# Performance work log

Hardware: AMD Instinct MI355X
Metric: run time of the kernel (lower is better)

The kernel has to match this reference:

```python
import jax, jax.numpy as jnp
import numpy as np

EPS = 1e-5  # BatchNorm eps (eval mode, running_mean=0, running_var=1)


def conv1x1(x, w):
    # x: [n,c,h,w], w: [o,c]
    return jnp.einsum('nchw,oc->nohw', x, w)


def bn_relu(x, s, b):
    scale = s / jnp.sqrt(1.0 + EPS)
    return jax.nn.relu(x * scale[None, :, None, None] + b[None, :, None, None])


def upsample_bilinear_ac(x, out_h, out_w):
    # nn.Upsample(mode='bilinear', align_corners=True)
    n, c, h, w = x.shape
    ys = jnp.linspace(0.0, h - 1.0, out_h)
    xs = jnp.linspace(0.0, w - 1.0, out_w)
    y0 = jnp.floor(ys).astype(jnp.int32)
    y1 = jnp.minimum(y0 + 1, h - 1)
    x0 = jnp.floor(xs).astype(jnp.int32)
    x1 = jnp.minimum(x0 + 1, w - 1)
    wy = (ys - y0)[None, None, :, None]
    wx = (xs - x0)[None, None, None, :]
    rows = x[:, :, y0, :] * (1.0 - wy) + x[:, :, y1, :] * wy
    return rows[:, :, :, x0] * (1.0 - wx) + rows[:, :, :, x1] * wx


def to_patches(x, ph, pw):
    # [n,c,H,W] -> [n,c,P,L], P = (H//ph)*(W//pw) patches, L = ph*pw pixels
    n, c, H, W = x.shape
    gh, gw = H // ph, W // pw
    return x.reshape(n, c, gh, ph, gw, pw).transpose(0, 1, 2, 4, 3, 5).reshape(n, c, gh * gw, ph * pw)


def from_patches(x, H, W, ph, pw):
    n, c, P, L = x.shape
    gh, gw = H // ph, W // pw
    return x.reshape(n, c, gh, gw, ph, pw).transpose(0, 1, 2, 4, 3, 5).reshape(n, c, H, W)


def patch_attention(q, k, v, ph, pw, H, W):
    qp = to_patches(q, ph, pw)
    kp = to_patches(k, ph, pw)
    vp = to_patches(v, ph, pw)
    # patch-vs-patch similarity, contracted over pixels within a patch
    sim = jax.nn.sigmoid(jnp.einsum('ncpl,ncql->ncpq', qp, kp))
    # sim1 (mean over key patches) + sim2 (mean over query patches), both [n,c,P,1]
    gate = sim.mean(axis=3, keepdims=True) + sim.mean(axis=2)[..., None]
    return from_patches(gate * vp, H, W, ph, pw)


def setup_inputs() -> dict:
    key = jax.random.key(0)
    ks = jax.random.split(key, 20)
    N, Ch, Cl, neck = 8, 256, 512, 64
    H = W = 128
    Hs = Ws = 32
    sc = 0.05
    return {
        'branch0_feats': jax.random.normal(ks[0], (N, Ch, H, W), jnp.float32),
        'other_feats': jax.random.normal(ks[1], (N, Cl, Hs, Ws), jnp.float32),
        'wq1': jax.random.normal(ks[2], (neck, Ch), jnp.float32) * sc,
        'bnq1_s': jax.random.uniform(ks[3], (neck,), jnp.float32, 0.5, 1.5),
        'bnq1_b': jax.random.normal(ks[4], (neck,), jnp.float32) * 0.1,
        'wk1': jax.random.normal(ks[5], (neck, Cl), jnp.float32) * sc,
        'bnk1_s': jax.random.uniform(ks[6], (neck,), jnp.float32, 0.5, 1.5),
        'bnk1_b': jax.random.normal(ks[7], (neck,), jnp.float32) * 0.1,
        'wv1': jax.random.normal(ks[8], (neck, Ch), jnp.float32) * sc,
        'wq2': jax.random.normal(ks[9], (neck, Ch), jnp.float32) * sc,
        'bnq2_s': jax.random.uniform(ks[10], (neck,), jnp.float32, 0.5, 1.5),
        'bnq2_b': jax.random.normal(ks[11], (neck,), jnp.float32) * 0.1,
        'wk2': jax.random.normal(ks[12], (neck, Cl), jnp.float32) * sc,
        'bnk2_s': jax.random.uniform(ks[13], (neck,), jnp.float32, 0.5, 1.5),
        'bnk2_b': jax.random.normal(ks[14], (neck,), jnp.float32) * 0.1,
        'wz': jax.random.normal(ks[15], (Ch, 2 * neck), jnp.float32) * sc,
        'alpha': jax.random.uniform(ks[16], (1,), jnp.float32),
        'gamma': jax.random.uniform(ks[17], (1,), jnp.float32),
    }


def reference(branch0_feats, other_feats, wq1, bnq1_s, bnq1_b, wk1, bnk1_s, bnk1_b, wv1,
              wq2, bnq2_s, bnq2_b, wk2, bnk2_s, bnk2_b, wz, alpha, gamma):
    _, _, H, W = branch0_feats.shape
    _, _, Hs, Ws = other_feats.shape

    value = conv1x1(branch0_feats, wv1)
    query = bn_relu(conv1x1(branch0_feats, wq1), bnq1_s, bnq1_b)
    key = upsample_bilinear_ac(bn_relu(conv1x1(other_feats, wk1), bnk1_s, bnk1_b), H, W)

    half = query.shape[1] // 2
    # scale 1: patches of size (Hs, Ws)
    ctx0 = patch_attention(query[:, :half], key[:, :half], value[:, :half], Hs, Ws, H, W)
    # scale 2: patches of size (Hs//2, Ws//2)
    ctx2 = patch_attention(query[:, half:], key[:, half:], value[:, half:], Hs // 2, Ws // 2, H, W)

    # dense per-pixel sigmoid gating branch
    query2 = bn_relu(conv1x1(branch0_feats, wq2), bnq2_s, bnq2_b)
    key2 = upsample_bilinear_ac(bn_relu(conv1x1(other_feats, wk2), bnk2_s, bnk2_b), H, W)
    ctx3 = value * jax.nn.sigmoid(query2 * key2)

    context = jnp.concatenate([alpha[0] * jnp.concatenate([ctx0, ctx2], axis=1),
                               gamma[0] * ctx3], axis=1)
    return conv1x1(context, wz)
```

## Files before the change

### kernel.cpp

```cpp
#include <hip/hip_runtime.h>
#include <hip/hip_bf16.h>
#include <math.h>
#include <stdint.h>

#define N_    8
#define CH    256
#define CL    512
#define NECK  64
#define H_    128
#define W_    128
#define HW    16384
#define HWS   1024
#define EPSB  1e-5f
#define SC31  (31.0f/127.0f)

typedef unsigned short ushort_t;
typedef __attribute__((ext_vector_type(8))) short bf16x8;
typedef __attribute__((ext_vector_type(4))) float f32x4;

union bfpack { ushort_t u[8]; bf16x8 v; };

__device__ __forceinline__ float sigmoidf_(float x){ return 1.0f/(1.0f + __expf(-x)); }

__device__ __forceinline__ ushort_t f2bf(float x){
    union { __hip_bfloat16 h; ushort_t u; } cv;
    cv.h = __float2bfloat16(x);
    return cv.u;
}
__device__ __forceinline__ uint32_t pack2(float lo, float hi){
    return (uint32_t)f2bf(lo) | ((uint32_t)f2bf(hi) << 16);
}
__device__ __forceinline__ float bf2f(ushort_t b){
    union { uint32_t u; float f; } v; v.u = ((uint32_t)b) << 16;
    return v.f;
}

__global__ __launch_bounds__(512) void k_phase1(
    const float* __restrict__ x,
    const float* __restrict__ xo,
    const float* __restrict__ wv1, const float* __restrict__ wq1, const float* __restrict__ wq2,
    const float* __restrict__ wk1, const float* __restrict__ wk2,
    const float* __restrict__ s1, const float* __restrict__ b1,
    const float* __restrict__ s2, const float* __restrict__ b2,
    const float* __restrict__ sk1, const float* __restrict__ bk1,
    const float* __restrict__ sk2, const float* __restrict__ bk2,
    const float* __restrict__ wz,
    ushort_t* __restrict__ value, ushort_t* __restrict__ query, ushort_t* __restrict__ query2,
    float* __restrict__ k1s, float* __restrict__ k2s, ushort_t* __restrict__ Wzb)
{
    __shared__ __align__(16) char smem[40960];
    int blk = blockIdx.x;
    int t = threadIdx.x;

    if (blk >= 1088){
        int i = (blk - 1088)*2048 + t*4;
        float4 f = *(const float4*)(wz + i);
        *(uint2*)(Wzb + i) = make_uint2(pack2(f.x,f.y), pack2(f.z,f.w));
        return;
    }

    int lane = t & 63, w8 = t >> 6;
    int wm = w8 >> 1, wn = w8 & 1;
    int r16 = lane & 15;
    float inv = rsqrtf(1.0f + EPSB);

    if (blk >= 1024){
        ushort_t* At = (ushort_t*)smem;
        ushort_t* Bt = (ushort_t*)(smem + 16384);
        int b = blk - 1024;
        int n = b >> 3, pix0 = (b & 7) << 7;
        f32x4 acc[2][4];
        #pragma unroll
        for (int m=0;m<2;m++)
            #pragma unroll
            for (int nn=0;nn<4;nn++) acc[m][nn] = (f32x4){0.f,0.f,0.f,0.f};

        const float* xb = xo + (size_t)n*CL*HWS + pix0;
        float va[8], vb[8];
        {
            const float* xc = xb + (size_t)(8*w8)*HWS;
            #pragma unroll
            for (int j=0;j<8;j++){
                va[j] = xc[(size_t)j*HWS + lane];
                vb[j] = xc[(size_t)j*HWS + 64 + lane];
            }
        }
        int oo = t >> 3, c8 = t & 7;
        for (int kt=0; kt<8; ++kt){
            int c0 = kt*64;
            const float* ws0 = wk1 + (size_t)oo*CL + c0 + c8*8;
            const float* ws1 = wk2 + (size_t)oo*CL + c0 + c8*8;
            float4 a00 = *(const float4*)ws0, a01 = *(const float4*)(ws0+4);
            float4 a10 = *(const float4*)ws1, a11 = *(const float4*)(ws1+4);
            uint32_t pa[4], pb[4];
            #pragma unroll
            for (int j=0;j<4;j++){
                pa[j] = pack2(va[2*j], va[2*j+1]);
                pb[j] = pack2(vb[2*j], vb[2*j+1]);
            }
            int offA = (lane*128 + w8*16) ^ ((lane&7)<<4);
            int offB = ((lane+64)*128 + w8*16) ^ ((lane&7)<<4);
            *(uint4*)((char*)Bt + offA) = make_uint4(pa[0],pa[1],pa[2],pa[3]);
            *(uint4*)((char*)Bt + offB) = make_uint4(pb[0],pb[1],pb[2],pb[3]);
            {
                int off0 = (oo*128 + c8*16) ^ ((oo&7)<<4);
                int off1 = ((64+oo)*128 + c8*16) ^ ((oo&7)<<4);
                *(uint4*)((char*)At + off0) = make_uint4(pack2(a00.x,a00.y),pack2(a00.z,a00.w),
                                                         pack2(a01.x,a01.y),pack2(a01.z,a01.w));
                *(uint4*)((char*)At + off1) = make_uint4(pack2(a10.x,a10.y),pack2(a10.z,a10.w),
                                                         pack2(a11.x,a11.y),pack2(a11.z,a11.w));
            }
            __syncthreads();
            if (kt < 7){
                const float* xc = xb + (size_t)((kt+1)*64 + 8*w8)*HWS;
                #pragma unroll
                for (int j=0;j<8;j++){
                    va[j] = xc[(size_t)j*HWS + lane];
                    vb[j] = xc[(size_t)j*HWS + 64 + lane];
                }
            }
            #pragma unroll
            for (int ks=0; ks<2; ++ks){
                bf16x8 a[2], bfr[4];
                #pragma unroll
                for (int m=0;m<2;m++){
                    int row = wm*32 + m*16 + r16;
                    int off = (row*128 + ks*64 + (lane>>4)*16) ^ ((row&7)<<4);
                    a[m] = *(const bf16x8*)((const char*)At + off);
                }
                #pragma unroll
                for (int nn=0;nn<4;nn++){
                    int row = wn*64 + nn*16 + r16;
                    int off = (row*128 + ks*64 + (lane>>4)*16) ^ ((row&7)<<4);
                    bfr[nn] = *(const bf16x8*)((const char*)Bt + off);
                }
                #pragma unroll
                for (int m=0;m<2;m++)
                    #pragma unroll
                    for (int nn=0;nn<4;nn++)
                        acc[m][nn] = __builtin_amdgcn_mfma_f32_16x16x32_bf16(a[m], bfr[nn], acc[m][nn], 0, 0, 0);
            }
            __syncthreads();
        }
        #pragma unroll
        for (int m=0;m<2;m++){
            int obase = wm*32 + m*16 + ((lane>>4)<<2);
            #pragma unroll
            for (int r=0;r<4;r++){
                int o = obase + r;
                int oc = o & 63;
                float sc = ((o<64) ? sk1[oc] : sk2[oc]) * inv;
                float bb =  (o<64) ? bk1[oc] : bk2[oc];
                float* dst = ((o<64) ? k1s : k2s) + ((size_t)n*NECK + oc)*HWS + pix0;
                #pragma unroll
                for (int nn=0;nn<4;nn++){
                    int px = wn*64 + nn*16 + r16;
                    dst[px] = fmaxf(fmaf(acc[m][nn][r], sc, bb), 0.f);
                }
            }
        }
        return;
    }

    ushort_t* At = (ushort_t*)smem;
    ushort_t* Bt = (ushort_t*)(smem + 24576);
    int n = blk >> 7;
    int pix0 = (blk & 127) << 7;

    f32x4 acc[3][4];
    #pragma unroll
    for (int m=0;m<3;m++)
        #pragma unroll
        for (int nn=0;nn<4;nn++) acc[m][nn] = (f32x4){0.f,0.f,0.f,0.f};

    const float* xb = x + (size_t)n*CH*HW + pix0;
    float va[8], vb[8];
    {
        const float* xc = xb + (size_t)(8*w8)*HW;
        #pragma unroll
        for (int j=0;j<8;j++){
            va[j] = xc[(size_t)j*HW + lane];
            vb[j] = xc[(size_t)j*HW + 64 + lane];
        }
    }
    int oo = t >> 3, c8 = t & 7;
    for (int kt=0; kt<4; ++kt){
        int c0 = kt*64;
        const float* ws0 = wv1 + (size_t)oo*CH + c0 + c8*8;
        const float* ws1 = wq1 + (size_t)oo*CH + c0 + c8*8;
        const float* ws2 = wq2 + (size_t)oo*CH + c0 + c8*8;
        float4 a00 = *(const float4*)ws0, a01 = *(const float4*)(ws0+4);
        float4 a10 = *(const float4*)ws1, a11 = *(const float4*)(ws1+4);
        float4 a20 = *(const float4*)ws2, a21 = *(const float4*)(ws2+4);
        uint32_t pa[4], pb[4];
        #pragma unroll
        for (int j=0;j<4;j++){
            pa[j] = pack2(va[2*j], va[2*j+1]);
            pb[j] = pack2(vb[2*j], vb[2*j+1]);
        }
        int c2 = w8*16;
        int offA = (lane*128 + c2) ^ ((lane&7)<<4);
        int offB = ((lane+64)*128 + c2) ^ ((lane&7)<<4);
        *(uint4*)((char*)Bt + offA) = make_uint4(pa[0],pa[1],pa[2],pa[3]);
        *(uint4*)((char*)Bt + offB) = make_uint4(pb[0],pb[1],pb[2],pb[3]);
        {
            int swz = (oo&7)<<4;
            int off0 = ((oo     )*128 + c8*16) ^ swz;
            int off1 = ((oo + 64)*128 + c8*16) ^ swz;
            int off2 = ((oo +128)*128 + c8*16) ^ swz;
            *(uint4*)((char*)At + off0) = make_uint4(pack2(a00.x,a00.y),pack2(a00.z,a00.w),
                                                     pack2(a01.x,a01.y),pack2(a01.z,a01.w));
            *(uint4*)((char*)At + off1) = make_uint4(pack2(a10.x,a10.y),pack2(a10.z,a10.w),
                                                     pack2(a11.x,a11.y),pack2(a11.z,a11.w));
            *(uint4*)((char*)At + off2) = make_uint4(pack2(a20.x,a20.y),pack2(a20.z,a20.w),
                                                     pack2(a21.x,a21.y),pack2(a21.z,a21.w));
        }
        __syncthreads();
        if (kt < 3){
            const float* xc = xb + (size_t)((kt+1)*64 + 8*w8)*HW;
            #pragma unroll
            for (int j=0;j<8;j++){
                va[j] = xc[(size_t)j*HW + lane];
                vb[j] = xc[(size_t)j*HW + 64 + lane];
            }
        }
        #pragma unroll
        for (int ks=0; ks<2; ++ks){
            bf16x8 a[3], bfr[4];
            #pragma unroll
            for (int m=0;m<3;m++){
                int row = wm*48 + m*16 + r16;
                int off = (row*128 + ks*64 + (lane>>4)*16) ^ ((row&7)<<4);
                a[m] = *(const bf16x8*)((const char*)At + off);
            }
            #pragma unroll
            for (int nn=0;nn<4;nn++){
                int row = wn*64 + nn*16 + r16;
                int off = (row*128 + ks*64 + (lane>>4)*16) ^ ((row&7)<<4);
                bfr[nn] = *(const bf16x8*)((const char*)Bt + off);
            }
            #pragma unroll
            for (int m=0;m<3;m++)
                #pragma unroll
                for (int nn=0;nn<4;nn++)
                    acc[m][nn] = __builtin_amdgcn_mfma_f32_16x16x32_bf16(a[m], bfr[nn], acc[m][nn], 0, 0, 0);
        }
        __syncthreads();
    }
    #pragma unroll
    for (int m=0;m<3;m++){
        int obase = wm*48 + m*16 + ((lane>>4)<<2);
        #pragma unroll
        for (int r=0;r<4;r++){
            int o = obase + r;
            int grp = o >> 6, oc = o & 63;
            float sc = 1.f, bb = 0.f;
            ushort_t* dst;
            if (grp == 0) dst = value;
            else if (grp == 1){ sc = s1[oc]*inv; bb = b1[oc]; dst = query; }
            else              { sc = s2[oc]*inv; bb = b2[oc]; dst = query2; }
            #pragma unroll
            for (int nn=0;nn<4;nn++){
                int pix = pix0 + wn*64 + nn*16 + r16;
                float v = acc[m][nn][r];
                if (grp) v = fmaxf(fmaf(v, sc, bb), 0.f);
                dst[((size_t)(n*NECK + oc))*HW + pix] = f2bf(v);
            }
        }
    }
}

__global__ __launch_bounds__(256) void k_gates(
    const ushort_t* __restrict__ query, const float* __restrict__ k1small,
    float* __restrict__ gate1, float* __restrict__ gate2)
{
    __shared__ __align__(16) char smem[69632];
    int bid = blockIdx.x;
    int t = threadIdx.x;
    int lane = t & 63, wv = t >> 6;
    int r16 = lane & 15, g = lane >> 4;
    float* ksm = (float*)smem;
    ushort_t* qt = (ushort_t*)(smem + 4096);
    ushort_t* kt = (ushort_t*)(smem + 4096 + 32768);

    if (bid < 256){
        int n = bid >> 5, c = bid & 31;
        const float* ks = k1small + (size_t)(n*NECK + c)*HWS;
        #pragma unroll
        for (int i=0;i<4;i++) ksm[i*256+t] = ks[i*256+t];
        __syncthreads();
        const ushort_t* qb = query + (size_t)(n*NECK + c)*HW;
        #pragma unroll
        for (int i=0;i<8;i++){
            int task = i*256 + t;
            int p = task >> 7, c8 = task & 127;
            int ly = c8 >> 2, lx8 = (c8 & 3)*8;
            int h = (p>>2)*32 + ly, w = (p&3)*32 + lx8;
            bf16x8 qv = *(const bf16x8*)(qb + h*W_ + w);
            int off = (p*2048 + c8*16) ^ ((p&7)<<4);
            *(bf16x8*)((char*)qt + off) = qv;
            float yf = h*SC31; int y0=(int)yf; int y1=min(y0+1,31); float fy=yf-(float)y0;
            bfpack pk;
            #pragma unroll
            for (int j=0;j<8;j++){
                int ww = w + j;
                float xf = ww*SC31; int x0=(int)xf; int x1=min(x0+1,31); float fx=xf-(float)x0;
                float a=ksm[y0*32+x0], b=ksm[y0*32+x1], cc=ksm[y1*32+x0], d=ksm[y1*32+x1];
                float r0=a+(b-a)*fx, r1=cc+(d-cc)*fx;
                pk.u[j] = f2bf(r0 + (r1-r0)*fy);
            }
            *(bf16x8*)((char*)kt + off) = pk.v;
        }
        __syncthreads();
        f32x4 acc = (f32x4){0.f,0.f,0.f,0.f};
        #pragma unroll
        for (int k8=0; k8<8; ++k8){
            int l0 = wv*256 + k8*32 + g*8;
            int off = (r16*2048 + l0*2) ^ ((r16&7)<<4);
            bf16x8 av = *(const bf16x8*)((char*)qt + off);
            bf16x8 bv = *(const bf16x8*)((char*)kt + off);
            acc = __builtin_amdgcn_mfma_f32_16x16x32_bf16(av, bv, acc, 0, 0, 0);
        }
        __syncthreads();
        float* pw = (float*)smem;
        #pragma unroll
        for (int r=0;r<4;r++)
            pw[wv*256 + (g*4+r)*16 + r16] = acc[r];
        __syncthreads();
        float* simM = (float*)(smem + 4096);
        float s = pw[t] + pw[256+t] + pw[512+t] + pw[768+t];
        simM[t] = sigmoidf_(s);
        __syncthreads();
        if (t < 16){
            float rs=0.f, cs=0.f;
            #pragma unroll
            for (int q=0;q<16;q++) rs += simM[t*16+q];
            #pragma unroll
            for (int p=0;p<16;p++) cs += simM[p*16+t];
            gate1[(size_t)(n*32 + c)*16 + t] = (rs + cs) * (1.0f/16.0f);
        }
    } else {
        int b2 = bid - 256;
        int n = b2 >> 5, cl = b2 & 31, c = 32 + cl;
        const float* ks = k1small + (size_t)(n*NECK + c)*HWS;
        #pragma unroll
        for (int i=0;i<4;i++) ksm[i*256+t] = ks[i*256+t];
        __syncthreads();
        const ushort_t* qb = query + (size_t)(n*NECK + c)*HW;
        #pragma unroll
        for (int i=0;i<8;i++){
            int task = i*256 + t;
            int p = task >> 5, c8 = task & 31;
            int ly = c8 >> 1, lx8 = (c8 & 1)*8;
            int h = (p>>3)*16 + ly, w = (p&7)*16 + lx8;
            bf16x8 qv = *(const bf16x8*)(qb + h*W_ + w);
            int off = (p*512 + c8*16) ^ ((p&7)<<4);
            *(bf16x8*)((char*)qt + off) = qv;
            float yf = h*SC31; int y0=(int)yf; int y1=min(y0+1,31); float fy=yf-(float)y0;
            bfpack pk;
            #pragma unroll
            for (int j=0;j<8;j++){
                int ww = w + j;
                float xf = ww*SC31; int x0=(int)xf; int x1=min(x0+1,31); float fx=xf-(float)x0;
                float a=ksm[y0*32+x0], b=ksm[y0*32+x1], cc=ksm[y1*32+x0], d=ksm[y1*32+x1];
                float r0=a+(b-a)*fx, r1=cc+(d-cc)*fx;
                pk.u[j] = f2bf(r0 + (r1-r0)*fy);
            }
            *(bf16x8*)((char*)kt + off) = pk.v;
        }
        __syncthreads();
        f32x4 acc2[4];
        #pragma unroll
        for (int qc=0;qc<4;qc++) acc2[qc] = (f32x4){0.f,0.f,0.f,0.f};
        #pragma unroll
        for (int k8=0; k8<8; ++k8){
            int l0 = k8*32 + g*8;
            int offA = ((wv*16 + r16)*512 + l0*2) ^ ((r16&7)<<4);
            bf16x8 av = *(const bf16x8*)((char*)qt + offA);
            #pragma unroll
            for (int qc=0;qc<4;qc++){
                int offB = ((qc*16 + r16)*512 + l0*2) ^ ((r16&7)<<4);
                bf16x8 bv = *(const bf16x8*)((char*)kt + offB);
                acc2[qc] = __builtin_amdgcn_mfma_f32_16x16x32_bf16(av, bv, acc2[qc], 0, 0, 0);
            }
        }
        __syncthreads();
        float* simM = (float*)smem;
        #pragma unroll
        for (int qc=0;qc<4;qc++)
            #pragma unroll
            for (int r=0;r<4;r++){
                int p = wv*16 + g*4 + r, q = qc*16 + r16;
                simM[p*65 + q] = sigmoidf_(acc2[qc][r]);
            }
        __syncthreads();
        if (t < 64){
            float rs=0.f, cs=0.f;
            for (int q=0;q<64;q++) rs += simM[t*65 + q];
            for (int p=0;p<64;p++) cs += simM[p*65 + t];
            gate2[(size_t)(n*32 + cl)*64 + t] = (rs + cs) * (1.0f/64.0f);
        }
    }
}

__global__ __launch_bounds__(512, 4) void k_final_mfma(
    const ushort_t* __restrict__ value, const ushort_t* __restrict__ query2,
    const float* __restrict__ k2small,
    const float* __restrict__ gate1, const float* __restrict__ gate2,
    const ushort_t* __restrict__ Wzb,
    const float* __restrict__ alpha_p, const float* __restrict__ gamma_p,
    float* __restrict__ out)
{
    __shared__ __align__(16) char smem[59392];
    ushort_t* Ct = (ushort_t*)smem;
    float* g1s = (float*)(smem + 32768);
    float* g2s = (float*)(smem + 34816);
    float* k2r = (float*)(smem + 43008);
    int blk = blockIdx.x;
    int n = blk >> 7, h = blk & 127;
    int pix0 = h << 7;
    int t = threadIdx.x;
    int lane = t & 63;
    int wid = t >> 6;
    int wm = wid >> 1, wn = wid & 1;

    int px = t & 127, qd = t >> 7;
    const size_t vbase = (size_t)n*NECK*HW + pix0 + px;
    ushort_t vreg[16], qreg[16];
    #pragma unroll
    for (int i=0;i<16;i++){
        int c = qd*16 + i;
        vreg[i] = value [vbase + (size_t)c*HW];
        qreg[i] = query2[vbase + (size_t)c*HW];
    }

    float alpha = alpha_p[0], gamma = gamma_p[0];
    g1s[t & 511] = gate1[(size_t)n*512 + (t & 511)];
    #pragma unroll
    for (int i=0;i<4;i++) g2s[i*512 + t] = gate2[(size_t)n*2048 + i*512 + t];

    float yf = h * SC31;
    int y0 = (int)yf, y1 = min(y0+1, 31);
    float fy = yf - (float)y0;
    #pragma unroll
    for (int i=0;i<8;i++){
        int e = i*512 + t;
        int buf = e >> 11, c = (e >> 5) & 63, xx = e & 31;
        k2r[buf*2048 + c*32 + xx] = k2small[((size_t)n*NECK + c)*HWS + (buf ? y1 : y0)*32 + xx];
    }
    __syncthreads();

    float xf = px * SC31;
    int x0 = (int)xf, x1 = min(x0+1, 31);
    float fx = xf - (float)x0;
    int patch1 = (h>>5)*4 + (px>>5);
    int patch2 = (h>>4)*8 + (px>>4);
    #pragma unroll
    for (int j=0;j<2;j++){
        bfpack pk;
        #pragma unroll
        for (int i=0;i<8;i++){
            int ch = qd*16 + j*8 + i;
            float g = (ch < 32) ? g1s[ch*16 + patch1] : g2s[(ch-32)*64 + patch2];
            pk.u[i] = f2bf(alpha * g * bf2f(vreg[j*8+i]));
        }
        int off = (px*256 + qd*32 + j*16) ^ ((px&7)<<4);
        *(bf16x8*)((char*)Ct + off) = pk.v;
    }
    #pragma unroll
    for (int j=0;j<2;j++){
        bfpack pk;
        #pragma unroll
        for (int i=0;i<8;i++){
            int c = qd*16 + j*8 + i;
            float vv = bf2f(vreg[j*8+i]);
            float q2 = bf2f(qreg[j*8+i]);
            float r0 = k2r[c*32+x0];      r0 += (k2r[c*32+x1] - r0)*fx;
            float r1 = k2r[2048+c*32+x0]; r1 += (k2r[2048+c*32+x1] - r1)*fx;
            float kv = r0 + (r1 - r0)*fy;
            pk.u[i] = f2bf(gamma * vv * sigmoidf_(q2*kv));
        }
        int off = (px*256 + 128 + qd*32 + j*16) ^ ((px&7)<<4);
        *(bf16x8*)((char*)Ct + off) = pk.v;
    }
    __syncthreads();

    f32x4 acc[4][4];
    #pragma unroll
    for (int m=0;m<4;m++)
        #pragma unroll
        for (int nn=0;nn<4;nn++) acc[m][nn] = (f32x4){0.f,0.f,0.f,0.f};
    #pragma unroll
    for (int ks=0; ks<4; ++ks){
        bf16x8 a[4], b[4];
        #pragma unroll
        for (int m=0;m<4;m++){
            int row = wm*64 + m*16 + (lane&15);
            a[m] = *(const bf16x8*)(Wzb + row*128 + ks*32 + (lane>>4)*8);
        }
        #pragma unroll
        for (int nn=0;nn<4;nn++){
            int row = wn*64 + nn*16 + (lane&15);
            int off = (row*256 + ks*64 + (lane>>4)*16) ^ ((row&7)<<4);
            b[nn] = *(const bf16x8*)((const char*)Ct + off);
        }
        #pragma unroll
        for (int m=0;m<4;m++)
            #pragma unroll
            for (int nn=0;nn<4;nn++)
                acc[m][nn] = __builtin_amdgcn_mfma_f32_16x16x32_bf16(a[m], b[nn], acc[m][nn], 0, 0, 0);
    }

    #pragma unroll
    for (int m=0;m<4;m++){
        int obase = wm*64 + m*16 + ((lane>>4)<<2);
        #pragma unroll
        for (int r=0;r<4;r++){
            int o = obase + r;
            float* dst = out + ((size_t)(n*CH + o))*HW + pix0 + wn*64 + (lane&15);
            #pragma unroll
            for (int nn=0;nn<4;nn++)
                dst[nn*16] = acc[m][nn][r];
        }
    }
}

extern "C" void kernel_launch(void* const* d_in, const int* in_sizes, int n_in,
                              void* d_out, int out_size, void* d_ws, size_t ws_size,
                              hipStream_t stream) {
    const float* x0  = (const float*)d_in[0];
    const float* xo  = (const float*)d_in[1];
    const float* wq1 = (const float*)d_in[2];
    const float* s1  = (const float*)d_in[3];
    const float* b1  = (const float*)d_in[4];
    const float* wk1 = (const float*)d_in[5];
    const float* sk1 = (const float*)d_in[6];
    const float* bk1 = (const float*)d_in[7];
    const float* wv1 = (const float*)d_in[8];
    const float* wq2 = (const float*)d_in[9];
    const float* s2  = (const float*)d_in[10];
    const float* b2  = (const float*)d_in[11];
    const float* wk2 = (const float*)d_in[12];
    const float* sk2 = (const float*)d_in[13];
    const float* bk2 = (const float*)d_in[14];
    const float* wz  = (const float*)d_in[15];
    const float* alp = (const float*)d_in[16];
    const float* gam = (const float*)d_in[17];

    ushort_t* value  = (ushort_t*)d_ws;
    ushort_t* query  = value  + 8388608;
    ushort_t* query2 = query  + 8388608;
    float*    k1s    = (float*)(query2 + 8388608);
    float*    k2s    = k1s + 524288;
    float*    g1     = k2s + 524288;
    float*    g2     = g1 + 4096;
    ushort_t* Wzb    = (ushort_t*)(g2 + 16384);

    k_phase1<<<dim3(1104), dim3(512), 0, stream>>>(
        x0, xo, wv1, wq1, wq2, wk1, wk2, s1, b1, s2, b2, sk1, bk1, sk2, bk2, wz,
        value, query, query2, k1s, k2s, Wzb);
    k_gates<<<dim3(512), dim3(256), 0, stream>>>(query, k1s, g1, g2);
    k_final_mfma<<<dim3(1024), dim3(512), 0, stream>>>(value, query2, k2s, g1, g2, Wzb,
                                                       alp, gam, (float*)d_out);
}
```

Before: 127.8 us.

## Stage full-K activation tile in LDS once, load weights directly to registers

```diff
diff --git a/kernel.cpp b/kernel.cpp
--- a/kernel.cpp
+++ b/kernel.cpp
@@ -18,7 +18,8 @@
 typedef __attribute__((ext_vector_type(8))) short bf16x8;
 typedef __attribute__((ext_vector_type(4))) float f32x4;
 
-union bfpack { ushort_t u[8]; bf16x8 v; };
+union bfpack  { ushort_t u[8]; bf16x8 v; };
+union bfpack4 { uint32_t u[4]; bf16x8 v; };
 
 __device__ __forceinline__ float sigmoidf_(float x){ return 1.0f/(1.0f + __expf(-x)); }
 
@@ -35,7 +36,7 @@
     return v.f;
 }
 
-__global__ __launch_bounds__(512) void k_phase1(
+__global__ __launch_bounds__(512, 4) void k_phase1(
     const float* __restrict__ x,
     const float* __restrict__ xo,
     const float* __restrict__ wv1, const float* __restrict__ wq1, const float* __restrict__ wq2,
@@ -48,26 +49,18 @@
     ushort_t* __restrict__ value, ushort_t* __restrict__ query, ushort_t* __restrict__ query2,
     float* __restrict__ k1s, float* __restrict__ k2s, ushort_t* __restrict__ Wzb)
 {
-    __shared__ __align__(16) char smem[40960];
+    __shared__ __align__(16) char smem[65536];
     int blk = blockIdx.x;
     int t = threadIdx.x;
-
-    if (blk >= 1088){
-        int i = (blk - 1088)*2048 + t*4;
-        float4 f = *(const float4*)(wz + i);
-        *(uint2*)(Wzb + i) = make_uint2(pack2(f.x,f.y), pack2(f.z,f.w));
-        return;
-    }
-
     int lane = t & 63, w8 = t >> 6;
-    int wm = w8 >> 1, wn = w8 & 1;
     int r16 = lane & 15;
     float inv = rsqrtf(1.0f + EPSB);
 
-    if (blk >= 1024){
+    if (blk < 64){
         ushort_t* At = (ushort_t*)smem;
         ushort_t* Bt = (ushort_t*)(smem + 16384);
-        int b = blk - 1024;
+        int wm = w8 >> 1, wn = w8 & 1;
+        int b = blk;
         int n = b >> 3, pix0 = (b & 7) << 7;
         f32x4 acc[2][4];
         #pragma unroll
@@ -162,10 +155,38 @@
         return;
     }
 
-    ushort_t* At = (ushort_t*)smem;
-    ushort_t* Bt = (ushort_t*)(smem + 24576);
-    int n = blk >> 7;
-    int pix0 = (blk & 127) << 7;
+    if (blk < 80){
+        int i = (blk - 64)*2048 + t*4;
+        float4 f = *(const float4*)(wz + i);
+        *(uint2*)(Wzb + i) = make_uint2(pack2(f.x,f.y), pack2(f.z,f.w));
+        return;
+    }
+
+    ushort_t* Bt = (ushort_t*)smem;
+    int tile = blk - 80;
+    int n = tile >> 7;
+    int pix0 = (tile & 127) << 7;
+    int wm = w8 >> 1, wn = w8 & 1;
+
+    {
+        int px = t & 127, chg = t >> 7;
+        const float* xc = x + (size_t)n*CH*HW + (size_t)(chg*64)*HW + pix0 + px;
+        #pragma unroll
+        for (int pass=0; pass<4; ++pass){
+            float v[16];
+            #pragma unroll
+            for (int j=0;j<16;j++) v[j] = xc[(size_t)(pass*16 + j)*HW];
+            uint32_t p[8];
+            #pragma unroll
+            for (int j=0;j<8;j++) p[j] = pack2(v[2*j], v[2*j+1]);
+            int base = px*512 + chg*128 + pass*32;
+            int o0 = base ^ ((px&7)<<4);
+            int o1 = (base + 16) ^ ((px&7)<<4);
+            *(uint4*)((char*)Bt + o0) = make_uint4(p[0],p[1],p[2],p[3]);
+            *(uint4*)((char*)Bt + o1) = make_uint4(p[4],p[5],p[6],p[7]);
+        }
+    }
+    __syncthreads();
 
     f32x4 acc[3][4];
     #pragma unroll
@@ -173,80 +194,41 @@
         #pragma unroll
         for (int nn=0;nn<4;nn++) acc[m][nn] = (f32x4){0.f,0.f,0.f,0.f};
 
-    const float* xb = x + (size_t)n*CH*HW + pix0;
-    float va[8], vb[8];
-    {
-        const float* xc = xb + (size_t)(8*w8)*HW;
-        #pragma unroll
-        for (int j=0;j<8;j++){
-            va[j] = xc[(size_t)j*HW + lane];
-            vb[j] = xc[(size_t)j*HW + 64 + lane];
-        }
-    }
-    int oo = t >> 3, c8 = t & 7;
-    for (int kt=0; kt<4; ++kt){
-        int c0 = kt*64;
-        const float* ws0 = wv1 + (size_t)oo*CH + c0 + c8*8;
-        const float* ws1 = wq1 + (size_t)oo*CH + c0 + c8*8;
-        const float* ws2 = wq2 + (size_t)oo*CH + c0 + c8*8;
-        float4 a00 = *(const float4*)ws0, a01 = *(const float4*)(ws0+4);
-        float4 a10 = *(const float4*)ws1, a11 = *(const float4*)(ws1+4);
-        float4 a20 = *(const float4*)ws2, a21 = *(const float4*)(ws2+4);
-        uint32_t pa[4], pb[4];
-        #pragma unroll
-        for (int j=0;j<4;j++){
-            pa[j] = pack2(va[2*j], va[2*j+1]);
-            pb[j] = pack2(vb[2*j], vb[2*j+1]);
-        }
-        int c2 = w8*16;
-        int offA = (lane*128 + c2) ^ ((lane&7)<<4);
-        int offB = ((lane+64)*128 + c2) ^ ((lane&7)<<4);
-        *(uint4*)((char*)Bt + offA) = make_uint4(pa[0],pa[1],pa[2],pa[3]);
-        *(uint4*)((char*)Bt + offB) = make_uint4(pb[0],pb[1],pb[2],pb[3]);
-        {
-            int swz = (oo&7)<<4;
-            int off0 = ((oo     )*128 + c8*16) ^ swz;
-            int off1 = ((oo + 64)*128 + c8*16) ^ swz;
-            int off2 = ((oo +128)*128 + c8*16) ^ swz;
-            *(uint4*)((char*)At + off0) = make_uint4(pack2(a00.x,a00.y),pack2(a00.z,a00.w),
-                                                     pack2(a01.x,a01.y),pack2(a01.z,a01.w));
-            *(uint4*)((char*)At + off1) = make_uint4(pack2(a10.x,a10.y),pack2(a10.z,a10.w),
-                                                     pack2(a11.x,a11.y),pack2(a11.z,a11.w));
-            *(uint4*)((char*)At + off2) = make_uint4(pack2(a20.x,a20.y),pack2(a20.z,a20.w),
-                                                     pack2(a21.x,a21.y),pack2(a21.z,a21.w));
-        }
-        __syncthreads();
-        if (kt < 3){
-            const float* xc = xb + (size_t)((kt+1)*64 + 8*w8)*HW;
-            #pragma unroll
-            for (int j=0;j<8;j++){
-                va[j] = xc[(size_t)j*HW + lane];
-                vb[j] = xc[(size_t)j*HW + 64 + lane];
-            }
-        }
-        #pragma unroll
-        for (int ks=0; ks<2; ++ks){
-            bf16x8 a[3], bfr[4];
-            #pragma unroll
-            for (int m=0;m<3;m++){
-                int row = wm*48 + m*16 + r16;
-                int off = (row*128 + ks*64 + (lane>>4)*16) ^ ((row&7)<<4);
-                a[m] = *(const bf16x8*)((const char*)At + off);
-            }
-            #pragma unroll
-            for (int nn=0;nn<4;nn++){
-                int row = wn*64 + nn*16 + r16;
-                int off = (row*128 + ks*64 + (lane>>4)*16) ^ ((row&7)<<4);
-                bfr[nn] = *(const bf16x8*)((const char*)Bt + off);
-            }
-            #pragma unroll
-            for (int m=0;m<3;m++)
-                #pragma unroll
-                for (int nn=0;nn<4;nn++)
-                    acc[m][nn] = __builtin_amdgcn_mfma_f32_16x16x32_bf16(a[m], bfr[nn], acc[m][nn], 0, 0, 0);
-        }
-        __syncthreads();
-    }
+    const float* abase[3];
+    #pragma unroll
+    for (int m=0;m<3;m++){
+        int row = wm*48 + m*16 + r16;
+        const float* wsrc = (row < 64)  ? (wv1 + (size_t)row*CH)
+                          : (row < 128) ? (wq1 + (size_t)(row-64)*CH)
+                                        : (wq2 + (size_t)(row-128)*CH);
+        abase[m] = wsrc + (lane>>4)*8;
+    }
+
+    #pragma unroll
+    for (int ks=0; ks<8; ++ks){
+        bf16x8 a[3], b[4];
+        #pragma unroll
+        for (int m=0;m<3;m++){
+            const float* s = abase[m] + ks*32;
+            float4 f0 = *(const float4*)s, f1 = *(const float4*)(s+4);
+            bfpack4 pk;
+            pk.u[0] = pack2(f0.x,f0.y); pk.u[1] = pack2(f0.z,f0.w);
+            pk.u[2] = pack2(f1.x,f1.y); pk.u[3] = pack2(f1.z,f1.w);
+            a[m] = pk.v;
+        }
+        #pragma unroll
+        for (int nn=0;nn<4;nn++){
+            int row = wn*64 + nn*16 + r16;
+            int off = (row*512 + ks*64 + (lane>>4)*16) ^ ((row&7)<<4);
+            b[nn] = *(const bf16x8*)((const char*)Bt + off);
+        }
+        #pragma unroll
+        for (int m=0;m<3;m++)
+            #pragma unroll
+            for (int nn=0;nn<4;nn++)
+                acc[m][nn] = __builtin_amdgcn_mfma_f32_16x16x32_bf16(a[m], b[nn], acc[m][nn], 0, 0, 0);
+    }
+
     #pragma unroll
     for (int m=0;m<3;m++){
         int obase = wm*48 + m*16 + ((lane>>4)<<2);
```

Measured after the change: 145.7 us. 1.14x slower.
